# Kernel optimization log

Hardware: AMD Instinct MI355X
Metric: run time of the kernel (lower is better)

Reference implementation:

```python
import jax, jax.numpy as jnp
import numpy as np
from functools import partial

T, B, OBS, H, A = 512, 256, 128, 64, 16


def ste_sign(x):
    # forward: sign(x); backward: identity (straight-through estimator)
    return x + jax.lax.stop_gradient(jnp.sign(x) - x)


def setup_inputs() -> dict:
    key = jax.random.key(0)
    ks = jax.random.split(key, 20)
    def lin_w(k, fan_in, fan_out, std=1.0):
        return (jax.random.normal(k, (fan_out, fan_in), jnp.float32) * (std / np.sqrt(fan_in)))
    inp = {
        "x": jax.random.normal(ks[0], (T * B, OBS), jnp.float32),
        "gru_state": jnp.zeros((1, B, H), jnp.float32),
        "done": (jax.random.uniform(ks[1], (T * B,)) < 0.05).astype(jnp.float32),
        # GRU params (PyTorch layout: [3H, in], gate order r,z,n)
        "w_ih": lin_w(ks[2], OBS, 3 * H),
        "w_hh": lin_w(ks[3], H, 3 * H),
        "b_ih": jnp.zeros((3 * H,), jnp.float32),
        "b_hh": jnp.zeros((3 * H,), jnp.float32),
        # actor MLP: (H+OBS)->64->64->A
        "a_w1": lin_w(ks[4], H + OBS, 64), "a_b1": jnp.zeros((64,), jnp.float32),
        "a_w2": lin_w(ks[5], 64, 64),      "a_b2": jnp.zeros((64,), jnp.float32),
        "a_w3": lin_w(ks[6], 64, A, std=0.01), "a_b3": jnp.zeros((A,), jnp.float32),
        # critic MLP: (H+OBS)->64->64->1
        "c_w1": lin_w(ks[7], H + OBS, 64), "c_b1": jnp.zeros((64,), jnp.float32),
        "c_w2": lin_w(ks[8], 64, 64),      "c_b2": jnp.zeros((64,), jnp.float32),
        "c_w3": lin_w(ks[9], 64, 1),       "c_b3": jnp.zeros((1,), jnp.float32),
    }
    return inp


def _gru_scan(x, gru_state, done, w_ih, w_hh, b_ih, b_hh):
    # x: [T*B, OBS], gru_state: [1, B, H], done: [T*B]
    bsz = gru_state.shape[1]
    xs = x.reshape(-1, bsz, x.shape[-1])       # [T, B, OBS]
    ds = done.reshape(-1, bsz)                 # [T, B]
    # input-to-hidden gates for the whole sequence in one GEMM
    gi_all = jnp.einsum("tbi,gi->tbg", xs, w_ih) + b_ih   # [T, B, 3H]
    h0 = gru_state[0]                          # [B, H]

    def step(h, inputs):
        gi, d = inputs
        h = (1.0 - d)[:, None] * h             # done-masking of carried state
        gh = h @ w_hh.T + b_hh                 # [B, 3H]
        i_r, i_z, i_n = jnp.split(gi, 3, axis=-1)
        h_r, h_z, h_n = jnp.split(gh, 3, axis=-1)
        r = jax.nn.sigmoid(i_r + h_r)
        z = jax.nn.sigmoid(i_z + h_z)
        n = jnp.tanh(i_n + r * h_n)
        h_new = (1.0 - z) * n + z * h
        # quantized == 1: carried state is STE-sign quantized
        h_carry = ste_sign(h_new)
        out = ste_sign(h_new)                  # per-step output is also quantized
        return h_carry, out

    h_last, outs = jax.lax.scan(step, h0, (gi_all, ds))
    hidden = outs.reshape(-1, h0.shape[-1])    # [T*B, H]
    return hidden, h_last[None]                # [T*B, H], [1, B, H]


def _mlp(y, w1, b1, w2, b2, w3, b3):
    y = jnp.tanh(y @ w1.T + b1)
    y = jnp.tanh(y @ w2.T + b2)
    return y @ w3.T + b3


def reference(x, gru_state, done, w_ih, w_hh, b_ih, b_hh,
              a_w1, a_b1, a_w2, a_b2, a_w3, a_b3,
              c_w1, c_b1, c_w2, c_b2, c_w3, c_b3):
    hidden, new_state = _gru_scan(x, gru_state, done, w_ih, w_hh, b_ih, b_hh)
    cat = jnp.concatenate([hidden, x], axis=1)            # input_to_actor=True
    logits = _mlp(cat, a_w1, a_b1, a_w2, a_b2, a_w3, a_b3)
    value = _mlp(cat, c_w1, c_b1, c_w2, c_b2, c_w3, c_b3)
    return logits, value, new_state
```

## Files before the change

kernel.cpp:

```cpp
#include <hip/hip_runtime.h>
#include <math.h>

#define TT 512
#define BB 256
#define OBSZ 128
#define HH 64
#define G3 192
#define NROW (TT*BB)
#define SEGCAP 128
#define WT 768

__device__ __forceinline__ float fast_rcp(float x) {
    return __builtin_amdgcn_rcpf(x);
}
__device__ __forceinline__ float tanh_fast(float x) {
    float xc = fminf(fmaxf(x, -20.0f), 20.0f);
    float e2 = __expf(2.0f * xc);
    return (e2 - 1.0f) * fast_rcp(e2 + 1.0f);
}

__global__ __launch_bounds__(64, 1)
void seg_build_kernel(const float* __restrict__ done,
                      unsigned int* __restrict__ segs, int* __restrict__ segcnt)
{
    const int b = blockIdx.x;
    const int l = threadIdx.x;
    __shared__ int starts[SEGCAP];
    __shared__ int scnt_s;

    unsigned int m = 0;
    #pragma unroll
    for (int k = 0; k < 8; ++k) {
        int t = l*8 + k;
        float d = done[(size_t)t*BB + b];
        if (t > 0 && d != 0.f) m |= (1u << k);
    }
    int cnt = __popc(m) + (l == 0 ? 1 : 0);
    int inc = cnt;
    for (int s = 1; s < 64; s <<= 1) {
        int v = __shfl_up(inc, s);
        if (l >= s) inc += v;
    }
    int total = __shfl(inc, 63);
    int w = inc - cnt;
    if (l == 0 && w < SEGCAP) starts[w++] = 0;
    #pragma unroll
    for (int k = 0; k < 8; ++k)
        if (m & (1u << k)) { if (w < SEGCAP) starts[w] = l*8 + k; ++w; }
    if (l == 0) scnt_s = (total < SEGCAP) ? total : SEGCAP;
    __syncthreads();

    const int n = scnt_s;
    for (int i = l; i < n; i += 64) {
        int t0 = starts[i];
        int t1 = (i+1 < n) ? starts[i+1] : TT;
        int li = t1 - t0;
        int rank = 0;
        for (int j = 0; j < n; ++j) {
            int s0 = starts[j];
            int s1 = (j+1 < n) ? starts[j+1] : TT;
            int lj = s1 - s0;
            rank += (int)((lj > li) || (lj == li && j < i));
        }
        segs[(size_t)b*SEGCAP + rank] = (unsigned int)t0 | ((unsigned int)li << 16);
    }
    if (l == 0) segcnt[b] = n;
}

__global__ __launch_bounds__(256, 3)
void seg_scan_kernel(const float* __restrict__ gi_ws, const float* __restrict__ h0,
                     const float* __restrict__ done,
                     const float* __restrict__ w_hh, const float* __restrict__ b_hh,
                     const unsigned int* __restrict__ segs, const int* __restrict__ segcnt,
                     signed char* __restrict__ hidden, float* __restrict__ state_out)
{
    const int b  = blockIdx.x;
    const int si = blockIdx.y;
    if (si >= segcnt[b]) return;
    const unsigned int sg = segs[(size_t)b*SEGCAP + si];
    const int t0  = (int)(sg & 0xffffu);
    const int len = (int)(sg >> 16);
    const int tau = threadIdx.x;

    __shared__ __align__(16) float whsT[16*WT];
    __shared__ __align__(16) float hb[HH];
    __shared__ __align__(16) float srz[2*HH];
    __shared__ __align__(16) float sinb[HH];
    __shared__ __align__(16) float shnb[HH];

    #pragma unroll
    for (int i = 0; i < 12; ++i) {
        int idx = tau + i*256;
        int g  = idx % G3;
        int j4 = idx / G3;
        *(float4*)&whsT[j4*WT + g*4] = *(const float4*)&w_hh[g*HH + j4*4];
    }

    float bh = 0.f, gp0 = 0.f, gp1 = 0.f;
    if (tau < G3) {
        bh  = b_hh[tau];
        gp0 = gi_ws[((size_t)t0*BB + b)*G3 + tau];
        if (len > 1) gp1 = gi_ws[((size_t)(t0+1)*BB + b)*G3 + tau];
    } else {
        const int hl = tau - G3;
        float hi = 0.f;
        if (t0 == 0) {
            float d0 = done[0*BB + b];
            hi = (1.0f - d0) * h0[b*HH + hl];
        }
        hb[hl] = hi;
    }
    __syncthreads();

    for (int tt = 0; tt < len; ++tt) {
        const int t = t0 + tt;
        if (tau < G3) {
            float gi = gp0;
            gp0 = gp1;
            if (tt+2 < len) gp1 = gi_ws[((size_t)(t+2)*BB + b)*G3 + tau];
            int hvi = __float_as_int(hb[tau & 63]);
            float a0=0.f, a1=0.f, a2=0.f, a3=0.f;
            #pragma unroll
            for (int j4 = 0; j4 < HH/4; ++j4) {
                float4 wv = *(const float4*)&whsT[j4*WT + tau*4];
                a0 = fmaf(__int_as_float(__builtin_amdgcn_readlane(hvi, 4*j4+0)), wv.x, a0);
                a1 = fmaf(__int_as_float(__builtin_amdgcn_readlane(hvi, 4*j4+1)), wv.y, a1);
                a2 = fmaf(__int_as_float(__builtin_amdgcn_readlane(hvi, 4*j4+2)), wv.z, a2);
                a3 = fmaf(__int_as_float(__builtin_amdgcn_readlane(hvi, 4*j4+3)), wv.w, a3);
            }
            float gh = bh + ((a0+a1)+(a2+a3));
            if (tau < 2*HH) srz[tau] = gi + gh;
            else { sinb[tau-2*HH] = gi; shnb[tau-2*HH] = gh; }
        }
        __syncthreads();

        if (tau >= G3) {
            const int hl = tau - G3;
            float sr = srz[hl];
            float sz = srz[HH + hl];
            float r = 1.0f / (1.0f + expf(-sr));
            float z = 1.0f / (1.0f + expf(-sz));
            float n = tanhf(sinb[hl] + r * shnb[hl]);
            float hm = hb[hl];
            float hnew = (1.0f - z)*n + z*hm;
            float s = (hnew > 0.f) ? 1.f : ((hnew < 0.f) ? -1.f : 0.f);
            hidden[(size_t)(t*BB + b)*HH + hl] = (signed char)s;
            if (t == TT-1) state_out[b*HH + hl] = s;
            hb[hl] = s;
        }
        __syncthreads();
    }
}

__global__ __launch_bounds__(256, 2)
void gi_proj_kernel(const float* __restrict__ x,
                    const float* __restrict__ w_ih, const float* __restrict__ b_ih,
                    float* __restrict__ gi_ws)
{
    __shared__ __align__(16) float ws[G3*68];
    const int tid = threadIdx.x;
    const int q   = tid & 15;
    const int rp  = tid >> 4;
    const int rowb = blockIdx.x * 32;

    float bg[12];
    #pragma unroll
    for (int jj = 0; jj < 12; ++jj) bg[jj] = b_ih[q + 16*jj];

    float c0[12][2], c1[12][2], c2[12][2], c3[12][2];
    #pragma unroll
    for (int jj = 0; jj < 12; ++jj)
        #pragma unroll
        for (int r = 0; r < 2; ++r) { c0[jj][r]=0.f; c1[jj][r]=0.f; c2[jj][r]=0.f; c3[jj][r]=0.f; }

    #pragma unroll
    for (int half = 0; half < 2; ++half) {
        __syncthreads();
        #pragma unroll
        for (int i = 0; i < 12; ++i) {
            int idx = tid + i*256;
            int g = idx >> 4, k4 = idx & 15;
            *(float4*)&ws[g*68 + k4*4] =
                *(const float4*)&w_ih[(size_t)g*OBSZ + half*64 + k4*4];
        }
        __syncthreads();

        for (int kc = 0; kc < 8; ++kc) {
            float cv[2][8];
            #pragma unroll
            for (int r = 0; r < 2; ++r) {
                const float* xp = x + (size_t)(rowb + rp*2 + r)*OBSZ + half*64 + kc*8;
                float4 a = *(const float4*)xp;
                float4 c = *(const float4*)(xp + 4);
                cv[r][0]=a.x; cv[r][1]=a.y; cv[r][2]=a.z; cv[r][3]=a.w;
                cv[r][4]=c.x; cv[r][5]=c.y; cv[r][6]=c.z; cv[r][7]=c.w;
            }
            #pragma unroll
            for (int jj = 0; jj < 12; ++jj) {
                const float* wp = &ws[(q + 16*jj)*68 + kc*8];
                float4 w0 = *(const float4*)wp;
                float4 w1 = *(const float4*)(wp + 4);
                #pragma unroll
                for (int r = 0; r < 2; ++r) {
                    c0[jj][r] = fmaf(cv[r][0], w0.x, c0[jj][r]);
                    c1[jj][r] = fmaf(cv[r][1], w0.y, c1[jj][r]);
                    c2[jj][r] = fmaf(cv[r][2], w0.z, c2[jj][r]);
                    c3[jj][r] = fmaf(cv[r][3], w0.w, c3[jj][r]);
                    c0[jj][r] = fmaf(cv[r][4], w1.x, c0[jj][r]);
                    c1[jj][r] = fmaf(cv[r][5], w1.y, c1[jj][r]);
                    c2[jj][r] = fmaf(cv[r][6], w1.z, c2[jj][r]);
                    c3[jj][r] = fmaf(cv[r][7], w1.w, c3[jj][r]);
                }
            }
        }
    }

    #pragma unroll
    for (int r = 0; r < 2; ++r) {
        const size_t row = rowb + rp*2 + r;
        #pragma unroll
        for (int jj = 0; jj < 12; ++jj) {
            float o = bg[jj] + ((c0[jj][r]+c1[jj][r]) + (c2[jj][r]+c3[jj][r]));
            gi_ws[row*G3 + q + 16*jj] = o;
        }
    }
}

__global__ __launch_bounds__(256, 1)
void scan_kernel_fused(const float* __restrict__ x, const float* __restrict__ h0,
                       const float* __restrict__ done,
                       const float* __restrict__ w_ih, const float* __restrict__ w_hh,
                       const float* __restrict__ b_ih, const float* __restrict__ b_hh,
                       signed char* __restrict__ hidden, float* __restrict__ state_out)
{
    const int b   = blockIdx.x;
    const int tau = threadIdx.x;

    __shared__ __align__(16) float xb[2][OBSZ];
    __shared__ __align__(16) float hb[HH];
    __shared__ __align__(16) float srz[2*HH];
    __shared__ __align__(16) float sinb[HH];
    __shared__ __align__(16) float shnb[HH];

    float4 wi4[OBSZ/4];
    float4 wh4[HH/4];
    float bi = 0.f, bh = 0.f;
    if (tau < G3) {
        const float4* wip = (const float4*)(w_ih + tau*OBSZ);
        #pragma unroll
        for (int k4 = 0; k4 < OBSZ/4; ++k4) wi4[k4] = wip[k4];
        const float4* whp = (const float4*)(w_hh + tau*HH);
        #pragma unroll
        for (int j4 = 0; j4 < HH/4; ++j4) wh4[j4] = whp[j4];
        bi = b_ih[tau]; bh = b_hh[tau];
    } else {
        const int hl = tau - G3;
        const int k0 = hl*2;
        float2 v = *(const float2*)(x + (size_t)(0*BB + b)*OBSZ + k0);
        xb[0][k0] = v.x; xb[0][k0+1] = v.y;
        float d0 = done[0*BB + b];
        hb[hl] = (1.0f - d0) * h0[b*HH + hl];
    }
    __syncthreads();

    float dnext = 0.f;
    for (int t = 0; t < TT; ++t) {
        const int cur = t & 1, nxt = cur ^ 1;
        if (tau < G3) {
            const float4* hb4 = (const float4*)hb;
            float a0=0.f, a1=0.f, a2=0.f, a3=0.f;
            #pragma unroll
            for (int j4 = 0; j4 < HH/4; ++j4) {
                float4 hv = hb4[j4];
                a0 = fmaf(hv.x, wh4[j4].x, a0);
                a1 = fmaf(hv.y, wh4[j4].y, a1);
                a2 = fmaf(hv.z, wh4[j4].z, a2);
                a3 = fmaf(hv.w, wh4[j4].w, a3);
            }
            float gh = bh + ((a0+a1)+(a2+a3));
            const float4* xb4 = (const float4*)xb[cur];
            float g0=0.f, g1=0.f, g2=0.f, g3=0.f;
            #pragma unroll
            for (int k4 = 0; k4 < OBSZ/4; ++k4) {
                float4 xv = xb4[k4];
                g0 = fmaf(xv.x, wi4[k4].x, g0);
                g1 = fmaf(xv.y, wi4[k4].y, g1);
                g2 = fmaf(xv.z, wi4[k4].z, g2);
                g3 = fmaf(xv.w, wi4[k4].w, g3);
            }
            float gi = bi + ((g0+g1)+(g2+g3));
            if (tau < 2*HH) srz[tau] = gi + gh;
            else { sinb[tau-2*HH] = gi; shnb[tau-2*HH] = gh; }
        } else {
            const int hl = tau - G3;
            if (t+1 < TT) {
                const int k0 = hl*2;
                float2 xr = *(const float2*)(x + (size_t)((t+1)*BB + b)*OBSZ + k0);
                xb[nxt][k0] = xr.x; xb[nxt][k0+1] = xr.y;
                dnext = done[(t+1)*BB + b];
            }
        }
        __syncthreads();

        if (tau >= G3) {
            const int hl = tau - G3;
            float sr = srz[hl];
            float sz = srz[HH + hl];
            float r = 1.0f / (1.0f + expf(-sr));
            float z = 1.0f / (1.0f + expf(-sz));
            float n = tanhf(sinb[hl] + r * shnb[hl]);
            float hm = hb[hl];
            float hnew = (1.0f - z)*n + z*hm;
            float s = (hnew > 0.f) ? 1.f : ((hnew < 0.f) ? -1.f : 0.f);
            hidden[(size_t)(t*BB + b)*HH + hl] = (signed char)s;
            if (t == TT-1) state_out[b*HH + hl] = s;
            hb[hl] = (t+1 < TT && dnext != 0.f) ? 0.f : s;
        }
        __syncthreads();
    }
}

template<int NOUT>
__global__ __launch_bounds__(256, 2)
void mlp_kernel(const signed char* __restrict__ hidden, const float* __restrict__ x,
                const float* __restrict__ w1, const float* __restrict__ b1,
                const float* __restrict__ w2, const float* __restrict__ b2,
                const float* __restrict__ w3, const float* __restrict__ b3,
                float* __restrict__ out)
{
    __shared__ __align__(16) float wbuf[64*100];
    __shared__ __align__(16) float ybuf[128*68];
    const int tid = threadIdx.x;
    const int g   = tid >> 3;
    const int q   = tid & 7;

    float bv1[8], bv2[8];
    #pragma unroll
    for (int j = 0; j < 8; ++j) { bv1[j] = b1[q + 8*j]; bv2[j] = b2[q + 8*j]; }

    for (int chunk = 0; chunk < 2; ++chunk) {
        const int row0 = blockIdx.x*256 + chunk*128 + g*4;

        float acc[8][4];
        #pragma unroll
        for (int j = 0; j < 8; ++j)
            #pragma unroll
            for (int r = 0; r < 4; ++r) acc[j][r] = bv1[j];

        auto dot8 = [&](float (&cv)[4][8], int colbase) {
            #pragma unroll
            for (int j = 0; j < 8; ++j) {
                const float* wp = &wbuf[(q + 8*j)*100 + colbase];
                float4 w0 = *(const float4*)wp;
                float4 w1v = *(const float4*)(wp + 4);
                #pragma unroll
                for (int r = 0; r < 4; ++r) {
                    acc[j][r] = fmaf(cv[r][0], w0.x,  acc[j][r]);
                    acc[j][r] = fmaf(cv[r][1], w0.y,  acc[j][r]);
                    acc[j][r] = fmaf(cv[r][2], w0.z,  acc[j][r]);
                    acc[j][r] = fmaf(cv[r][3], w0.w,  acc[j][r]);
                    acc[j][r] = fmaf(cv[r][4], w1v.x, acc[j][r]);
                    acc[j][r] = fmaf(cv[r][5], w1v.y, acc[j][r]);
                    acc[j][r] = fmaf(cv[r][6], w1v.z, acc[j][r]);
                    acc[j][r] = fmaf(cv[r][7], w1v.w, acc[j][r]);
                }
            }
        };

        #pragma unroll
        for (int half = 0; half < 2; ++half) {
            __syncthreads();
            #pragma unroll
            for (int i = 0; i < 6; ++i) {
                int v = tid + i*256;
                int f = v / 24, k4 = v % 24;
                *(float4*)&wbuf[f*100 + k4*4] =
                    *(const float4*)&w1[f*G3 + half*96 + k4*4];
            }
            __syncthreads();

            if (half == 0) {
                for (int kc = 0; kc < 8; ++kc) {
                    float cv[4][8];
                    #pragma unroll
                    for (int r = 0; r < 4; ++r) {
                        uint2 hv = *(const uint2*)(hidden + (size_t)(row0+r)*HH + kc*8);
                        cv[r][0] = (float)(signed char)(hv.x);
                        cv[r][1] = (float)(signed char)(hv.x >> 8);
                        cv[r][2] = (float)(signed char)(hv.x >> 16);
                        cv[r][3] = (float)(signed char)(hv.x >> 24);
                        cv[r][4] = (float)(signed char)(hv.y);
                        cv[r][5] = (float)(signed char)(hv.y >> 8);
                        cv[r][6] = (float)(signed char)(hv.y >> 16);
                        cv[r][7] = (float)(signed char)(hv.y >> 24);
                    }
                    dot8(cv, kc*8);
                }
                for (int kc = 0; kc < 4; ++kc) {
                    float cv[4][8];
                    #pragma unroll
                    for (int r = 0; r < 4; ++r) {
                        const float* xp = x + (size_t)(row0+r)*OBSZ + kc*8;
                        float4 a = *(const float4*)xp;
                        float4 c = *(const float4*)(xp + 4);
                        cv[r][0]=a.x; cv[r][1]=a.y; cv[r][2]=a.z; cv[r][3]=a.w;
                        cv[r][4]=c.x; cv[r][5]=c.y; cv[r][6]=c.z; cv[r][7]=c.w;
                    }
                    dot8(cv, 64 + kc*8);
                }
            } else {
                for (int kc = 0; kc < 12; ++kc) {
                    float cv[4][8];
                    #pragma unroll
                    for (int r = 0; r < 4; ++r) {
                        const float* xp = x + (size_t)(row0+r)*OBSZ + 32 + kc*8;
                        float4 a = *(const float4*)xp;
                        float4 c = *(const float4*)(xp + 4);
                        cv[r][0]=a.x; cv[r][1]=a.y; cv[r][2]=a.z; cv[r][3]=a.w;
                        cv[r][4]=c.x; cv[r][5]=c.y; cv[r][6]=c.z; cv[r][7]=c.w;
                    }
                    dot8(cv, kc*8);
                }
            }
        }

        #pragma unroll
        for (int j = 0; j < 8; ++j)
            #pragma unroll
            for (int r = 0; r < 4; ++r)
                ybuf[(g*4+r)*68 + q + 8*j] = tanh_fast(acc[j][r]);
        __syncthreads();

        #pragma unroll
        for (int i = 0; i < 4; ++i) {
            int v = tid + i*256;
            int f = v >> 4, k4 = v & 15;
            *(float4*)&wbuf[f*68 + k4*4] = *(const float4*)&w2[f*HH + k4*4];
        }
        __syncthreads();

        float acc2[8][4];
        #pragma unroll
        for (int j = 0; j < 8; ++j)
            #pragma unroll
            for (int r = 0; r < 4; ++r) acc2[j][r] = bv2[j];

        for (int kc = 0; kc < 8; ++kc) {
            float cv[4][8];
            #pragma unroll
            for (int r = 0; r < 4; ++r) {
                const float* yp = &ybuf[(g*4+r)*68 + kc*8];
                float4 a = *(const float4*)yp;
                float4 c = *(const float4*)(yp + 4);
                cv[r][0]=a.x; cv[r][1]=a.y; cv[r][2]=a.z; cv[r][3]=a.w;
                cv[r][4]=c.x; cv[r][5]=c.y; cv[r][6]=c.z; cv[r][7]=c.w;
            }
            #pragma unroll
            for (int j = 0; j < 8; ++j) {
                const float* wp = &wbuf[(q + 8*j)*68 + kc*8];
                float4 w0 = *(const float4*)wp;
                float4 w1v = *(const float4*)(wp + 4);
                #pragma unroll
                for (int r = 0; r < 4; ++r) {
                    acc2[j][r] = fmaf(cv[r][0], w0.x,  acc2[j][r]);
                    acc2[j][r] = fmaf(cv[r][1], w0.y,  acc2[j][r]);
                    acc2[j][r] = fmaf(cv[r][2], w0.z,  acc2[j][r]);
                    acc2[j][r] = fmaf(cv[r][3], w0.w,  acc2[j][r]);
                    acc2[j][r] = fmaf(cv[r][4], w1v.x, acc2[j][r]);
                    acc2[j][r] = fmaf(cv[r][5], w1v.y, acc2[j][r]);
                    acc2[j][r] = fmaf(cv[r][6], w1v.z, acc2[j][r]);
                    acc2[j][r] = fmaf(cv[r][7], w1v.w, acc2[j][r]);
                }
            }
        }
        __syncthreads();

        #pragma unroll
        for (int j = 0; j < 8; ++j)
            #pragma unroll
            for (int r = 0; r < 4; ++r)
                ybuf[(g*4+r)*68 + q + 8*j] = tanh_fast(acc2[j][r]);
        if (tid < NOUT*16) {
            int f = tid >> 4, k4 = tid & 15;
            *(float4*)&wbuf[f*68 + k4*4] = *(const float4*)&w3[f*HH + k4*4];
        }
        __syncthreads();

        #pragma unroll
        for (int oo = 0; oo < (NOUT + 7)/8; ++oo) {
            const int o = q + 8*oo;
            if (o < NOUT) {
                #pragma unroll
                for (int r = 0; r < 4; ++r) {
                    const float* yp = &ybuf[(g*4+r)*68];
                    const float* wp = &wbuf[o*68];
                    float s0=0.f, s1=0.f, s2=0.f, s3=0.f;
                    #pragma unroll
                    for (int k4 = 0; k4 < 16; ++k4) {
                        float4 yv = *(const float4*)(yp + k4*4);
                        float4 wv = *(const float4*)(wp + k4*4);
                        s0 = fmaf(yv.x, wv.x, s0);
                        s1 = fmaf(yv.y, wv.y, s1);
                        s2 = fmaf(yv.z, wv.z, s2);
                        s3 = fmaf(yv.w, wv.w, s3);
                    }
                    out[(size_t)(row0+r)*NOUT + o] = b3[o] + ((s0+s1)+(s2+s3));
                }
            }
        }
        __syncthreads();
    }
}

extern "C" void kernel_launch(void* const* d_in, const int* in_sizes, int n_in,
                              void* d_out, int out_size, void* d_ws, size_t ws_size,
                              hipStream_t stream) {
    const float* x     = (const float*)d_in[0];
    const float* h0    = (const float*)d_in[1];
    const float* done  = (const float*)d_in[2];
    const float* w_ih  = (const float*)d_in[3];
    const float* w_hh  = (const float*)d_in[4];
    const float* b_ih  = (const float*)d_in[5];
    const float* b_hh  = (const float*)d_in[6];
    const float* a_w1  = (const float*)d_in[7];
    const float* a_b1  = (const float*)d_in[8];
    const float* a_w2  = (const float*)d_in[9];
    const float* a_b2  = (const float*)d_in[10];
    const float* a_w3  = (const float*)d_in[11];
    const float* a_b3  = (const float*)d_in[12];
    const float* c_w1  = (const float*)d_in[13];
    const float* c_b1  = (const float*)d_in[14];
    const float* c_w2  = (const float*)d_in[15];
    const float* c_b2  = (const float*)d_in[16];
    const float* c_w3  = (const float*)d_in[17];
    const float* c_b3  = (const float*)d_in[18];

    float* out    = (float*)d_out;
    float* logits = out;
    float* value  = out + (size_t)NROW*16;
    float* state  = value + NROW;

    const size_t segs_bytes   = (size_t)BB * SEGCAP * sizeof(unsigned int);
    const size_t segcnt_bytes = (size_t)BB * sizeof(int);
    const size_t hidden_off   = segs_bytes + segcnt_bytes;
    const size_t hidden_bytes = (size_t)NROW * HH;
    const size_t gi_off       = hidden_off + hidden_bytes;
    const size_t gi_bytes     = (size_t)NROW * G3 * sizeof(float);

    if (ws_size >= gi_off + gi_bytes) {
        unsigned int* segs = (unsigned int*)d_ws;
        int* segcnt        = (int*)((char*)d_ws + segs_bytes);
        signed char* hidden = (signed char*)((char*)d_ws + hidden_off);
        float* gi_ws       = (float*)((char*)d_ws + gi_off);

        seg_build_kernel<<<BB, 64, 0, stream>>>(done, segs, segcnt);
        gi_proj_kernel<<<NROW/32, 256, 0, stream>>>(x, w_ih, b_ih, gi_ws);
        seg_scan_kernel<<<dim3(BB, SEGCAP), 256, 0, stream>>>(
            gi_ws, h0, done, w_hh, b_hh, segs, segcnt, hidden, state);
        mlp_kernel<16><<<512, 256, 0, stream>>>(hidden, x, a_w1, a_b1, a_w2, a_b2,
                                                a_w3, a_b3, logits);
        mlp_kernel<1><<<512, 256, 0, stream>>>(hidden, x, c_w1, c_b1, c_w2, c_b2,
                                               c_w3, c_b3, value);
    } else {
        signed char* hidden = (signed char*)d_ws;
        scan_kernel_fused<<<BB, 256, 0, stream>>>(x, h0, done, w_ih, w_hh,
                                                  b_ih, b_hh, hidden, state);
        mlp_kernel<16><<<512, 256, 0, stream>>>(hidden, x, a_w1, a_b1, a_w2, a_b2,
                                                a_w3, a_b3, logits);
        mlp_kernel<1><<<512, 256, 0, stream>>>(hidden, x, c_w1, c_b1, c_w2, c_b2,
                                               c_w3, c_b3, value);
    }
}
```

Before: 531.2 us.

## Run one GRU segment per wavefront with all gates per lane, no block barriers

The segmented scan kernel now assigns one independent segment to each 64-lane wavefront, four per block. Each lane computes the r, z and n recurrent dot products for its hidden unit, using readlane broadcasts of the register-held state, then applies the gate math itself. This removes the shared-memory exchanges and the two __syncthreads per timestep, and cuts the grid by four. Each lane does three times the FMAs and needs more registers. The input-projection kernel is also retiled to 4 rows by 6 columns per thread instead of 2 by 12, changing the register blocking.

```diff
diff --git a/kernel.cpp b/kernel.cpp
--- a/kernel.cpp
+++ b/kernel.cpp
@@ -8,7 +8,6 @@
 #define G3 192
 #define NROW (TT*BB)
 #define SEGCAP 128
-#define WT 768
 
 __device__ __forceinline__ float fast_rcp(float x) {
     return __builtin_amdgcn_rcpf(x);
@@ -74,81 +73,100 @@
                      const unsigned int* __restrict__ segs, const int* __restrict__ segcnt,
                      signed char* __restrict__ hidden, float* __restrict__ state_out)
 {
-    const int b  = blockIdx.x;
-    const int si = blockIdx.y;
-    if (si >= segcnt[b]) return;
+    const int b    = blockIdx.x;
+    const int scnt = segcnt[b];
+    const int si0  = blockIdx.y * 4;
+    if (si0 >= scnt) return;
+
+    __shared__ __align__(16) float ws[G3*68];
+
+    const int tid = threadIdx.x;
+    #pragma unroll
+    for (int i = 0; i < 12; ++i) {
+        int idx = tid + i*256;
+        int g = idx >> 4, k4 = idx & 15;
+        *(float4*)&ws[g*68 + k4*4] = *(const float4*)&w_hh[g*HH + k4*4];
+    }
+    __syncthreads();
+
+    const int wid = tid >> 6;
+    const int hl  = tid & 63;
+    const int si  = si0 + wid;
+    if (si >= scnt) return;
+
     const unsigned int sg = segs[(size_t)b*SEGCAP + si];
     const int t0  = (int)(sg & 0xffffu);
     const int len = (int)(sg >> 16);
-    const int tau = threadIdx.x;
-
-    __shared__ __align__(16) float whsT[16*WT];
-    __shared__ __align__(16) float hb[HH];
-    __shared__ __align__(16) float srz[2*HH];
-    __shared__ __align__(16) float sinb[HH];
-    __shared__ __align__(16) float shnb[HH];
-
-    #pragma unroll
-    for (int i = 0; i < 12; ++i) {
-        int idx = tau + i*256;
-        int g  = idx % G3;
-        int j4 = idx / G3;
-        *(float4*)&whsT[j4*WT + g*4] = *(const float4*)&w_hh[g*HH + j4*4];
-    }
-
-    float bh = 0.f, gp0 = 0.f, gp1 = 0.f;
-    if (tau < G3) {
-        bh  = b_hh[tau];
-        gp0 = gi_ws[((size_t)t0*BB + b)*G3 + tau];
-        if (len > 1) gp1 = gi_ws[((size_t)(t0+1)*BB + b)*G3 + tau];
+
+    const float bhr = b_hh[hl];
+    const float bhz = b_hh[64 + hl];
+    const float bhn = b_hh[128 + hl];
+
+    float h;
+    if (t0 == 0) {
+        float d0 = done[b];
+        h = (1.0f - d0) * h0[b*HH + hl];
     } else {
-        const int hl = tau - G3;
-        float hi = 0.f;
-        if (t0 == 0) {
-            float d0 = done[0*BB + b];
-            hi = (1.0f - d0) * h0[b*HH + hl];
-        }
-        hb[hl] = hi;
-    }
-    __syncthreads();
+        h = 0.f;
+    }
+
+    float gr0, gz0, gn0, gr1 = 0.f, gz1 = 0.f, gn1 = 0.f;
+    {
+        size_t o0 = ((size_t)t0*BB + b)*G3;
+        gr0 = gi_ws[o0 + hl]; gz0 = gi_ws[o0 + 64 + hl]; gn0 = gi_ws[o0 + 128 + hl];
+        if (len > 1) {
+            size_t o1 = ((size_t)(t0+1)*BB + b)*G3;
+            gr1 = gi_ws[o1 + hl]; gz1 = gi_ws[o1 + 64 + hl]; gn1 = gi_ws[o1 + 128 + hl];
+        }
+    }
+
+    const float* wr = &ws[hl*68];
+    const float* wz = &ws[(64 + hl)*68];
+    const float* wn = &ws[(128 + hl)*68];
 
     for (int tt = 0; tt < len; ++tt) {
         const int t = t0 + tt;
-        if (tau < G3) {
-            float gi = gp0;
-            gp0 = gp1;
-            if (tt+2 < len) gp1 = gi_ws[((size_t)(t+2)*BB + b)*G3 + tau];
-            int hvi = __float_as_int(hb[tau & 63]);
-            float a0=0.f, a1=0.f, a2=0.f, a3=0.f;
-            #pragma unroll
-            for (int j4 = 0; j4 < HH/4; ++j4) {
-                float4 wv = *(const float4*)&whsT[j4*WT + tau*4];
-                a0 = fmaf(__int_as_float(__builtin_amdgcn_readlane(hvi, 4*j4+0)), wv.x, a0);
-                a1 = fmaf(__int_as_float(__builtin_amdgcn_readlane(hvi, 4*j4+1)), wv.y, a1);
-                a2 = fmaf(__int_as_float(__builtin_amdgcn_readlane(hvi, 4*j4+2)), wv.z, a2);
-                a3 = fmaf(__int_as_float(__builtin_amdgcn_readlane(hvi, 4*j4+3)), wv.w, a3);
-            }
-            float gh = bh + ((a0+a1)+(a2+a3));
-            if (tau < 2*HH) srz[tau] = gi + gh;
-            else { sinb[tau-2*HH] = gi; shnb[tau-2*HH] = gh; }
-        }
-        __syncthreads();
-
-        if (tau >= G3) {
-            const int hl = tau - G3;
-            float sr = srz[hl];
-            float sz = srz[HH + hl];
-            float r = 1.0f / (1.0f + expf(-sr));
-            float z = 1.0f / (1.0f + expf(-sz));
-            float n = tanhf(sinb[hl] + r * shnb[hl]);
-            float hm = hb[hl];
-            float hnew = (1.0f - z)*n + z*hm;
-            float s = (hnew > 0.f) ? 1.f : ((hnew < 0.f) ? -1.f : 0.f);
-            hidden[(size_t)(t*BB + b)*HH + hl] = (signed char)s;
-            if (t == TT-1) state_out[b*HH + hl] = s;
-            hb[hl] = s;
-        }
-        __syncthreads();
+        const float gir = gr0, giz = gz0, gin = gn0;
+        gr0 = gr1; gz0 = gz1; gn0 = gn1;
+        if (tt + 2 < len) {
+            size_t o = ((size_t)(t+2)*BB + b)*G3;
+            gr1 = gi_ws[o + hl]; gz1 = gi_ws[o + 64 + hl]; gn1 = gi_ws[o + 128 + hl];
+        }
+
+        const int hvi = __float_as_int(h);
+        float ar0=0.f, ar1=0.f, ar2=0.f, ar3=0.f;
+        float az0=0.f, az1=0.f, az2=0.f, az3=0.f;
+        float an0=0.f, an1=0.f, an2=0.f, an3=0.f;
+        #pragma unroll
+        for (int j4 = 0; j4 < 16; ++j4) {
+            float4 wvr = *(const float4*)(wr + j4*4);
+            float4 wvz = *(const float4*)(wz + j4*4);
+            float4 wvn = *(const float4*)(wn + j4*4);
+            float h0f = __int_as_float(__builtin_amdgcn_readlane(hvi, 4*j4+0));
+            float h1f = __int_as_float(__builtin_amdgcn_readlane(hvi, 4*j4+1));
+            float h2f = __int_as_float(__builtin_amdgcn_readlane(hvi, 4*j4+2));
+            float h3f = __int_as_float(__builtin_amdgcn_readlane(hvi, 4*j4+3));
+            ar0 = fmaf(h0f, wvr.x, ar0);  ar1 = fmaf(h1f, wvr.y, ar1);
+            ar2 = fmaf(h2f, wvr.z, ar2);  ar3 = fmaf(h3f, wvr.w, ar3);
+            az0 = fmaf(h0f, wvz.x, az0);  az1 = fmaf(h1f, wvz.y, az1);
+            az2 = fmaf(h2f, wvz.z, az2);  az3 = fmaf(h3f, wvz.w, az3);
+            an0 = fmaf(h0f, wvn.x, an0);  an1 = fmaf(h1f, wvn.y, an1);
+            an2 = fmaf(h2f, wvn.z, an2);  an3 = fmaf(h3f, wvn.w, an3);
+        }
+        const float ghr = bhr + ((ar0+ar1)+(ar2+ar3));
+        const float ghz = bhz + ((az0+az1)+(az2+az3));
+        const float ghn = bhn + ((an0+an1)+(an2+an3));
+
+        const float sr = gir + ghr;
+        const float sz = giz + ghz;
+        float r = 1.0f / (1.0f + expf(-sr));
+        float z = 1.0f / (1.0f + expf(-sz));
+        float n = tanhf(gin + r * ghn);
+        float hnew = (1.0f - z)*n + z*h;
+        float s = (hnew > 0.f) ? 1.f : ((hnew < 0.f) ? -1.f : 0.f);
+        hidden[(size_t)(t*BB + b)*HH + hl] = (signed char)s;
+        if (t == TT-1) state_out[b*HH + hl] = s;
+        h = s;
     }
 }
 
@@ -158,20 +176,20 @@
                     float* __restrict__ gi_ws)
 {
     __shared__ __align__(16) float ws[G3*68];
-    const int tid = threadIdx.x;
-    const int q   = tid & 15;
-    const int rp  = tid >> 4;
+    const int tid  = threadIdx.x;
+    const int q    = tid & 31;
+    const int rp   = tid >> 5;
     const int rowb = blockIdx.x * 32;
 
-    float bg[12];
-    #pragma unroll
-    for (int jj = 0; jj < 12; ++jj) bg[jj] = b_ih[q + 16*jj];
-
-    float c0[12][2], c1[12][2], c2[12][2], c3[12][2];
-    #pragma unroll
-    for (int jj = 0; jj < 12; ++jj)
-        #pragma unroll
-        for (int r = 0; r < 2; ++r) { c0[jj][r]=0.f; c1[jj][r]=0.f; c2[jj][r]=0.f; c3[jj][r]=0.f; }
+    float bg[6];
+    #pragma unroll
+    for (int jj = 0; jj < 6; ++jj) bg[jj] = b_ih[q + 32*jj];
+
+    float c0[6][4], c1[6][4], c2[6][4], c3[6][4];
+    #pragma unroll
+    for (int jj = 0; jj < 6; ++jj)
+        #pragma unroll
+        for (int r = 0; r < 4; ++r) { c0[jj][r]=0.f; c1[jj][r]=0.f; c2[jj][r]=0.f; c3[jj][r]=0.f; }
 
     #pragma unroll
     for (int half = 0; half < 2; ++half) {
@@ -186,22 +204,22 @@
         __syncthreads();
 
         for (int kc = 0; kc < 8; ++kc) {
-            float cv[2][8];
-            #pragma unroll
-            for (int r = 0; r < 2; ++r) {
-                const float* xp = x + (size_t)(rowb + rp*2 + r)*OBSZ + half*64 + kc*8;
+            float cv[4][8];
+            #pragma unroll
+            for (int r = 0; r < 4; ++r) {
+                const float* xp = x + (size_t)(rowb + rp*4 + r)*OBSZ + half*64 + kc*8;
                 float4 a = *(const float4*)xp;
                 float4 c = *(const float4*)(xp + 4);
                 cv[r][0]=a.x; cv[r][1]=a.y; cv[r][2]=a.z; cv[r][3]=a.w;
                 cv[r][4]=c.x; cv[r][5]=c.y; cv[r][6]=c.z; cv[r][7]=c.w;
             }
             #pragma unroll
-            for (int jj = 0; jj < 12; ++jj) {
-                const float* wp = &ws[(q + 16*jj)*68 + kc*8];
+            for (int jj = 0; jj < 6; ++jj) {
+                const float* wp = &ws[(q + 32*jj)*68 + kc*8];
                 float4 w0 = *(const float4*)wp;
                 float4 w1 = *(const float4*)(wp + 4);
                 #pragma unroll
-                for (int r = 0; r < 2; ++r) {
+                for (int r = 0; r < 4; ++r) {
                     c0[jj][r] = fmaf(cv[r][0], w0.x, c0[jj][r]);
                     c1[jj][r] = fmaf(cv[r][1], w0.y, c1[jj][r]);
                     c2[jj][r] = fmaf(cv[r][2], w0.z, c2[jj][r]);
@@ -216,12 +234,12 @@
     }
 
     #pragma unroll
-    for (int r = 0; r < 2; ++r) {
-        const size_t row = rowb + rp*2 + r;
-        #pragma unroll
-        for (int jj = 0; jj < 12; ++jj) {
+    for (int r = 0; r < 4; ++r) {
+        const size_t row = rowb + rp*4 + r;
+        #pragma unroll
+        for (int jj = 0; jj < 6; ++jj) {
             float o = bg[jj] + ((c0[jj][r]+c1[jj][r]) + (c2[jj][r]+c3[jj][r]));
-            gi_ws[row*G3 + q + 16*jj] = o;
+            gi_ws[row*G3 + q + 32*jj] = o;
         }
     }
 }
@@ -555,7 +573,7 @@
 
         seg_build_kernel<<<BB, 64, 0, stream>>>(done, segs, segcnt);
         gi_proj_kernel<<<NROW/32, 256, 0, stream>>>(x, w_ih, b_ih, gi_ws);
-        seg_scan_kernel<<<dim3(BB, SEGCAP), 256, 0, stream>>>(
+        seg_scan_kernel<<<dim3(BB, SEGCAP/4), 256, 0, stream>>>(
             gi_ws, h0, done, w_hh, b_hh, segs, segcnt, hidden, state);
         mlp_kernel<16><<<512, 256, 0, stream>>>(hidden, x, a_w1, a_b1, a_w2, a_b2,
                                                 a_w3, a_b3, logits);
```

Result: slower. 1.027 ms (+93.4%).

## Pack two GRU segments per block sharing one staged w_hh copy

Applied to the files above, without the earlier changes.

The segmented GRU scan now runs two done-delimited segments per 512-thread block. Both share a single padded row-major copy of w_hh in LDS, which halves the per-segment weight staging and LDS footprint. The n-gate input projection is prefetched straight into registers by the gate threads instead of passing through shared memory. Segments come sorted by length, so the pair's loop runs for the first segment's length, and the shorter segment idles at barriers for those extra steps.

```diff
diff --git a/kernel.cpp b/kernel.cpp
--- a/kernel.cpp
+++ b/kernel.cpp
@@ -8,7 +8,6 @@
 #define G3 192
 #define NROW (TT*BB)
 #define SEGCAP 128
-#define WT 768
 
 __device__ __forceinline__ float fast_rcp(float x) {
     return __builtin_amdgcn_rcpf(x);
@@ -67,36 +66,45 @@
     if (l == 0) segcnt[b] = n;
 }
 
-__global__ __launch_bounds__(256, 3)
+__global__ __launch_bounds__(512, 6)
 void seg_scan_kernel(const float* __restrict__ gi_ws, const float* __restrict__ h0,
                      const float* __restrict__ done,
                      const float* __restrict__ w_hh, const float* __restrict__ b_hh,
                      const unsigned int* __restrict__ segs, const int* __restrict__ segcnt,
                      signed char* __restrict__ hidden, float* __restrict__ state_out)
 {
-    const int b  = blockIdx.x;
-    const int si = blockIdx.y;
-    if (si >= segcnt[b]) return;
-    const unsigned int sg = segs[(size_t)b*SEGCAP + si];
-    const int t0  = (int)(sg & 0xffffu);
-    const int len = (int)(sg >> 16);
-    const int tau = threadIdx.x;
-
-    __shared__ __align__(16) float whsT[16*WT];
-    __shared__ __align__(16) float hb[HH];
-    __shared__ __align__(16) float srz[2*HH];
-    __shared__ __align__(16) float sinb[HH];
-    __shared__ __align__(16) float shnb[HH];
-
-    #pragma unroll
-    for (int i = 0; i < 12; ++i) {
-        int idx = tau + i*256;
-        int g  = idx % G3;
-        int j4 = idx / G3;
-        *(float4*)&whsT[j4*WT + g*4] = *(const float4*)&w_hh[g*HH + j4*4];
-    }
+    const int b    = blockIdx.x;
+    const int scnt = segcnt[b];
+    const int si0  = blockIdx.y * 2;
+    if (si0 >= scnt) return;
+
+    __shared__ __align__(16) float ws[G3*68];
+    __shared__ __align__(16) float hb[2][HH];
+    __shared__ __align__(16) float srz[2][2*HH];
+    __shared__ __align__(16) float shnb[2][HH];
+
+    const int tid = threadIdx.x;
+    #pragma unroll
+    for (int i = 0; i < 6; ++i) {
+        int idx = tid + i*512;
+        int g = idx >> 4, k4 = idx & 15;
+        *(float4*)&ws[g*68 + k4*4] = *(const float4*)&w_hh[g*HH + k4*4];
+    }
+
+    const int grp = tid >> 8;
+    const int tau = tid & 255;
+    const int si  = si0 + grp;
+
+    int t0 = 0, len = 0;
+    if (si < scnt) {
+        unsigned int sg = segs[(size_t)b*SEGCAP + si];
+        t0  = (int)(sg & 0xffffu);
+        len = (int)(sg >> 16);
+    }
+    const int lmax = (int)(segs[(size_t)b*SEGCAP + si0] >> 16);
 
     float bh = 0.f, gp0 = 0.f, gp1 = 0.f;
+    float gn0 = 0.f, gn1 = 0.f;
     if (tau < G3) {
         bh  = b_hh[tau];
         gp0 = gi_ws[((size_t)t0*BB + b)*G3 + tau];
@@ -104,49 +112,55 @@
     } else {
         const int hl = tau - G3;
         float hi = 0.f;
-        if (t0 == 0) {
-            float d0 = done[0*BB + b];
+        if (len > 0 && t0 == 0) {
+            float d0 = done[b];
             hi = (1.0f - d0) * h0[b*HH + hl];
         }
-        hb[hl] = hi;
+        hb[grp][hl] = hi;
+        gn0 = gi_ws[((size_t)t0*BB + b)*G3 + 128 + hl];
+        if (len > 1) gn1 = gi_ws[((size_t)(t0+1)*BB + b)*G3 + 128 + hl];
     }
     __syncthreads();
 
-    for (int tt = 0; tt < len; ++tt) {
+    for (int tt = 0; tt < lmax; ++tt) {
         const int t = t0 + tt;
-        if (tau < G3) {
+        if (tau < G3 && tt < len) {
             float gi = gp0;
             gp0 = gp1;
             if (tt+2 < len) gp1 = gi_ws[((size_t)(t+2)*BB + b)*G3 + tau];
-            int hvi = __float_as_int(hb[tau & 63]);
+            int hvi = __float_as_int(hb[grp][tau & 63]);
+            const float* wrow = &ws[tau*68];
             float a0=0.f, a1=0.f, a2=0.f, a3=0.f;
             #pragma unroll
             for (int j4 = 0; j4 < HH/4; ++j4) {
-                float4 wv = *(const float4*)&whsT[j4*WT + tau*4];
+                float4 wv = *(const float4*)(wrow + j4*4);
                 a0 = fmaf(__int_as_float(__builtin_amdgcn_readlane(hvi, 4*j4+0)), wv.x, a0);
                 a1 = fmaf(__int_as_float(__builtin_amdgcn_readlane(hvi, 4*j4+1)), wv.y, a1);
                 a2 = fmaf(__int_as_float(__builtin_amdgcn_readlane(hvi, 4*j4+2)), wv.z, a2);
                 a3 = fmaf(__int_as_float(__builtin_amdgcn_readlane(hvi, 4*j4+3)), wv.w, a3);
             }
             float gh = bh + ((a0+a1)+(a2+a3));
-            if (tau < 2*HH) srz[tau] = gi + gh;
-            else { sinb[tau-2*HH] = gi; shnb[tau-2*HH] = gh; }
-        }
-        __syncthreads();
-
-        if (tau >= G3) {
+            if (tau < 2*HH) srz[grp][tau] = gi + gh;
+            else            shnb[grp][tau-2*HH] = gh;
+        }
+        __syncthreads();
+
+        if (tau >= G3 && tt < len) {
             const int hl = tau - G3;
-            float sr = srz[hl];
-            float sz = srz[HH + hl];
+            float gin = gn0;
+            gn0 = gn1;
+            if (tt+2 < len) gn1 = gi_ws[((size_t)(t+2)*BB + b)*G3 + 128 + hl];
+            float sr = srz[grp][hl];
+            float sz = srz[grp][HH + hl];
             float r = 1.0f / (1.0f + expf(-sr));
             float z = 1.0f / (1.0f + expf(-sz));
-            float n = tanhf(sinb[hl] + r * shnb[hl]);
-            float hm = hb[hl];
+            float n = tanhf(gin + r * shnb[grp][hl]);
+            float hm = hb[grp][hl];
             float hnew = (1.0f - z)*n + z*hm;
             float s = (hnew > 0.f) ? 1.f : ((hnew < 0.f) ? -1.f : 0.f);
             hidden[(size_t)(t*BB + b)*HH + hl] = (signed char)s;
             if (t == TT-1) state_out[b*HH + hl] = s;
-            hb[hl] = s;
+            hb[grp][hl] = s;
         }
         __syncthreads();
     }
@@ -555,7 +569,7 @@
 
         seg_build_kernel<<<BB, 64, 0, stream>>>(done, segs, segcnt);
         gi_proj_kernel<<<NROW/32, 256, 0, stream>>>(x, w_ih, b_ih, gi_ws);
-        seg_scan_kernel<<<dim3(BB, SEGCAP), 256, 0, stream>>>(
+        seg_scan_kernel<<<dim3(BB, SEGCAP/2), 512, 0, stream>>>(
             gi_ws, h0, done, w_hh, b_hh, segs, segcnt, hidden, state);
         mlp_kernel<16><<<512, 256, 0, stream>>>(hidden, x, a_w1, a_b1, a_w2, a_b2,
                                                 a_w3, a_b3, logits);
```

Result: faster. 515.1 us (-3.0%).
